# Performance work log

Measured on AMD Instinct MI355X. Metric: run time of the kernel, lower is better.

## Reference

```python
import jax, jax.numpy as jnp
import numpy as np

B, H, E, L = 2048, 4096, 8, 512
TAU = 1.0


def setup_inputs() -> dict:
    key = jax.random.key(0)
    k1, k2, k3, k4 = jax.random.split(key, 4)
    hidden = jax.random.normal(k1, (B, H), dtype=jnp.float32)
    envs = jax.random.normal(k2, (B, E), dtype=jnp.float32)
    idx = jnp.arange(B, dtype=jnp.int64)
    gumbel = jax.random.gumbel(k3, (B, E), dtype=jnp.float32)
    W = jax.random.normal(k4, (E, L, H), dtype=jnp.float32) * (1.0 / np.sqrt(H))
    return {"hidden": hidden, "envs": envs, "idx": idx, "gumbel": gumbel, "W": W}


def _hard_gumbel_softmax(log_probs, gumbel, tau):
    # F.gumbel_softmax(log_probs, tau=1, hard=True) with pre-sampled gumbel noise
    y_soft = jax.nn.softmax((log_probs + gumbel) / tau, axis=-1)
    y_hard = jax.nn.one_hot(jnp.argmax(y_soft, axis=-1), y_soft.shape[-1], dtype=y_soft.dtype)
    # straight-through estimator
    return y_hard + y_soft - jax.lax.stop_gradient(y_soft)


def reference(hidden, envs, idx, gumbel, W):
    # gating: env = gumbel_softmax(log_softmax(envs[idx]))  -> [B, E]
    log_probs = jax.nn.log_softmax(envs[idx], axis=-1)
    env = _hard_gumbel_softmax(log_probs, gumbel, TAU)
    # per-expert logits: [B, E, L]; fuses the per-sample python loop
    expert_logits = jnp.einsum("bh,elh->bel", hidden, W)
    # gating combine: [B, L]
    logits = jnp.einsum("be,bel->bl", env, expert_logits)
    # variance penalty over expert weights
    W_mean = jnp.mean(W, axis=0)  # [L, H]
    diff_sq = jnp.sum((W - W_mean[None]) ** 2, axis=(1, 2))  # ||W_e - W_mean||_2^2 per expert
    l1 = jnp.sum(jnp.abs(W), axis=(1, 2))                    # ||W_e||_1 per expert
    loss_penalty = jnp.mean(diff_sq / (l1 ** 2))
    return logits, loss_penalty
```

## Files before the change

### kernel.cpp

```cpp
#include <hip/hip_runtime.h>
#include <hip/hip_bf16.h>

constexpr int B = 2048, H = 4096, E = 8, L = 512;
constexpr int LH = L * H;

typedef float f4v __attribute__((ext_vector_type(4)));
typedef short short8 __attribute__((ext_vector_type(8)));

constexpr int BT = 64;
constexpr int LT = 128;
constexpr int KT = 32;
constexpr int SK = 4;
constexpr int RTMAX = 6;
constexpr int NITER = (H / SK) / KT;

constexpr int NGEMM = 4 * 2 * 4 * 4 * RTMAX;
constexpr int NPEN = 2048;

constexpr int NGRID = NGEMM + NPEN;

constexpr size_t WS_COUNTS = 0;
constexpr size_t WS_ACCUM = 32;
constexpr size_t WS_ROWLIST = 96;
constexpr size_t WS_ZERO_BYTES = 96;

using as1_u32 = const __attribute__((address_space(1))) unsigned int;
using as3_u32 = __attribute__((address_space(3))) unsigned int;

static __device__ __forceinline__ void dma16(const float* g, float* lds) {
  __builtin_amdgcn_global_load_lds((as1_u32*)g, (as3_u32*)lds, 16, 0, 0);
}

static __device__ __forceinline__ unsigned pk2(float a, float b) {
  __hip_bfloat162 p = __float22bfloat162_rn(make_float2(a, b));
  unsigned u;
  __builtin_memcpy(&u, &p, 4);
  return u;
}

static __device__ __forceinline__ short8 cvt8(f4v lo, f4v hi) {
  union { short8 s; unsigned u[4]; } r;
  r.u[0] = pk2(lo.x, lo.y);
  r.u[1] = pk2(lo.z, lo.w);
  r.u[2] = pk2(hi.x, hi.y);
  r.u[3] = pk2(hi.z, hi.w);
  return r.s;
}

__global__ void gating_kernel(const float* __restrict__ envs,
                              const float* __restrict__ gumbel,
                              int* __restrict__ counts,
                              int* __restrict__ row_list) {
  int b = blockIdx.x * blockDim.x + threadIdx.x;
  if (b >= B) return;
  float zmax = -1e30f;
  int am = 0;
#pragma unroll
  for (int e = 0; e < E; ++e) {
    float z = envs[b * E + e] + gumbel[b * E + e];
    if (z > zmax) { zmax = z; am = e; }
  }
  int pos = atomicAdd(&counts[am], 1);
  row_list[am * B + pos] = b;
}

__launch_bounds__(256, 3)
__global__ void fused_kernel(const float* __restrict__ hidden,
                             const float* __restrict__ W,
                             const int* __restrict__ counts,
                             const int* __restrict__ row_list,
                             float* __restrict__ out,
                             float* __restrict__ accum) {
  const int id = blockIdx.x;
  const int t = threadIdx.x;

  __shared__ __align__(16) float AshF[2][BT * KT];
  __shared__ __align__(16) float BshF[2][LT * KT];
  __shared__ int rlsh[BT];
  __shared__ float red[4][16];

  const int grp = id / 11;
  const int rem = id - grp * 11;
  const bool is_gemm = (rem < 3);

  if (!is_gemm) {
    const int p = (grp * 8 + (rem - 3)) * 256 + t;

    float4 w[E];
    float mx = 0.f, my = 0.f, mz = 0.f, mw = 0.f;
#pragma unroll
    for (int e = 0; e < E; ++e) {
      w[e] = *(const float4*)(W + (size_t)e * LH + (size_t)p * 4);
      mx += w[e].x; my += w[e].y; mz += w[e].z; mw += w[e].w;
    }
    mx *= 0.125f; my *= 0.125f; mz *= 0.125f; mw *= 0.125f;

    float vals[16];
#pragma unroll
    for (int e = 0; e < E; ++e) {
      float dx = w[e].x - mx, dy = w[e].y - my, dz = w[e].z - mz,
            dw = w[e].w - mw;
      vals[e] = dx * dx + dy * dy + dz * dz + dw * dw;
      vals[8 + e] =
          fabsf(w[e].x) + fabsf(w[e].y) + fabsf(w[e].z) + fabsf(w[e].w);
    }
#pragma unroll
    for (int k = 0; k < 16; ++k) {
      float v = vals[k];
      for (int off = 32; off > 0; off >>= 1) v += __shfl_xor(v, off);
      vals[k] = v;
    }
    const int wv = t >> 6, lane = t & 63;
    if (lane == 0) {
#pragma unroll
      for (int k = 0; k < 16; ++k) red[wv][k] = vals[k];
    }
    __syncthreads();
    if (t < 16) {
      atomicAdd(&accum[t], red[0][t] + red[1][t] + red[2][t] + red[3][t]);
    }
    return;
  }

  const int gidx = grp * 3 + rem;
  const int lt = gidx & 3;
  const int ep = (gidx >> 2) & 1;
  const int sk = (gidx >> 3) & 3;
  const int eh = (gidx >> 5) & 3;
  const int rt = gidx >> 7;
  const int e = eh * 2 + ep;

  const int cnt = counts[e];
  const int rbase = rt * BT;
  if (rbase >= cnt) return;
  const int lbase = lt * LT;

  if (t < BT) {
    int rr = rbase + t;
    rlsh[t] = row_list[e * B + (rr < cnt ? rr : (cnt - 1))];
  }
  __syncthreads();

  const float* Wp = W + (size_t)e * LH + (size_t)lbase * H;

  const int wave = t >> 6;
  const int lane = t & 63;
  const int quad = lane >> 4;
  const int l16 = lane & 15;
  const int wm = (wave >> 1) * 32;
  const int wn = (wave & 1) * 64;

  const int kbeg = sk * (H / SK);
  const int srow = lane >> 3;
  const int sblk = lane & 7;
  const int gblk = sblk ^ srow;

  const float* sp[6];
  float* sl[2][6];
#pragma unroll
  for (int i = 0; i < 6; ++i) {
    int g = wave * 6 + i;
    if (g < 8) {
      int rr = g * 8 + srow;
      sp[i] = hidden + (size_t)rlsh[rr] * H + kbeg + gblk * 4;
      sl[0][i] = &AshF[0][g * 8 * KT];
      sl[1][i] = &AshF[1][g * 8 * KT];
    } else {
      int rb = (g - 8) * 8 + srow;
      sp[i] = Wp + (size_t)rb * H + kbeg + gblk * 4;
      sl[0][i] = &BshF[0][(g - 8) * 8 * KT];
      sl[1][i] = &BshF[1][(g - 8) * 8 * KT];
    }
  }

  auto stage = [&](int buf) {
#pragma unroll
    for (int i = 0; i < 6; ++i) {
      dma16(sp[i], sl[buf][i]);
      sp[i] += KT;
    }
  };

  const int r7 = l16 & 7;
  const int slo = (2 * quad) ^ r7;
  const int shi = slo ^ 1;

  f4v acc[2][4] = {};

  stage(0);

  for (int it = 0; it < NITER; ++it) {
    const int buf = it & 1;
    __syncthreads();
    if (it + 1 < NITER) stage(buf ^ 1);

    short8 af[2], bf[4];
#pragma unroll
    for (int i = 0; i < 2; ++i) {
      int ra = wm + i * 16 + l16;
      f4v lo = *(const f4v*)&AshF[buf][ra * KT + slo * 4];
      f4v hi = *(const f4v*)&AshF[buf][ra * KT + shi * 4];
      af[i] = cvt8(lo, hi);
    }
#pragma unroll
    for (int j = 0; j < 4; ++j) {
      int rb = wn + j * 16 + l16;
      f4v lo = *(const f4v*)&BshF[buf][rb * KT + slo * 4];
      f4v hi = *(const f4v*)&BshF[buf][rb * KT + shi * 4];
      bf[j] = cvt8(lo, hi);
    }
#pragma unroll
    for (int i = 0; i < 2; ++i)
#pragma unroll
      for (int j = 0; j < 4; ++j)
        acc[i][j] =
            __builtin_amdgcn_mfma_f32_16x16x32_bf16(af[i], bf[j], acc[i][j],
                                                    0, 0, 0);
  }

#pragma unroll
  for (int i = 0; i < 2; ++i) {
#pragma unroll
    for (int j = 0; j < 4; ++j) {
#pragma unroll
      for (int reg = 0; reg < 4; ++reg) {
        int rloc = wm + i * 16 + quad * 4 + reg;
        if (rbase + rloc < cnt) {
          int bidx = rlsh[rloc];
          atomicAdd(&out[(size_t)bidx * L + lbase + wn + j * 16 + l16],
                    acc[i][j][reg]);
        }
      }
    }
  }
}

__global__ void finalize_kernel(const float* __restrict__ accum,
                                float* __restrict__ out) {
  if (threadIdx.x == 0) {
    float loss = 0.f;
#pragma unroll
    for (int e = 0; e < E; ++e) {
      float l1 = accum[8 + e];
      loss += accum[e] / (l1 * l1);
    }
    out[(size_t)B * L] = loss * 0.125f;
  }
}

extern "C" void kernel_launch(void* const* d_in, const int* in_sizes, int n_in,
                              void* d_out, int out_size, void* d_ws, size_t ws_size,
                              hipStream_t stream) {
  (void)in_sizes; (void)n_in; (void)ws_size;
  const float* hidden = (const float*)d_in[0];
  const float* envs   = (const float*)d_in[1];
  const float* gumbel = (const float*)d_in[3];
  const float* W      = (const float*)d_in[4];
  float* out = (float*)d_out;

  char* ws = (char*)d_ws;
  int*   counts   = (int*)(ws + WS_COUNTS);
  float* accum    = (float*)(ws + WS_ACCUM);
  int*   row_list = (int*)(ws + WS_ROWLIST);

  (void)hipMemsetAsync(d_ws, 0, WS_ZERO_BYTES, stream);
  (void)hipMemsetAsync(d_out, 0, (size_t)out_size * sizeof(float), stream);

  gating_kernel<<<dim3(B / 256), dim3(256), 0, stream>>>(envs, gumbel, counts,
                                                         row_list);

  fused_kernel<<<dim3(NGRID), dim3(256), 0, stream>>>(hidden, W, counts,
                                                      row_list, out, accum);

  finalize_kernel<<<dim3(1), dim3(64), 0, stream>>>(accum, out);
}
```

Measured before the change: 195.1 us.

## Enlarge GEMM row tile and stage bf16 operands in padded LDS via registers

```diff
diff --git a/kernel.cpp b/kernel.cpp
--- a/kernel.cpp
+++ b/kernel.cpp
@@ -7,28 +7,24 @@
 typedef float f4v __attribute__((ext_vector_type(4)));
 typedef short short8 __attribute__((ext_vector_type(8)));
 
-constexpr int BT = 64;
-constexpr int LT = 128;
-constexpr int KT = 32;
+constexpr int BT = 128, LT = 128, KT = 32;
 constexpr int SK = 4;
-constexpr int RTMAX = 6;
+constexpr int RTMAX = 3;
 constexpr int NITER = (H / SK) / KT;
+constexpr int ROWE = 40;
 
 constexpr int NGEMM = 4 * 2 * 4 * 4 * RTMAX;
 constexpr int NPEN = 2048;
-
 constexpr int NGRID = NGEMM + NPEN;
+
 
 constexpr size_t WS_COUNTS = 0;
 constexpr size_t WS_ACCUM = 32;
 constexpr size_t WS_ROWLIST = 96;
 constexpr size_t WS_ZERO_BYTES = 96;
 
-using as1_u32 = const __attribute__((address_space(1))) unsigned int;
-using as3_u32 = __attribute__((address_space(3))) unsigned int;
-
-static __device__ __forceinline__ void dma16(const float* g, float* lds) {
-  __builtin_amdgcn_global_load_lds((as1_u32*)g, (as3_u32*)lds, 16, 0, 0);
+static __device__ __forceinline__ void lgkm_barrier() {
+  __asm__ __volatile__("s_waitcnt lgkmcnt(0)\n\ts_barrier" ::: "memory");
 }
 
 static __device__ __forceinline__ unsigned pk2(float a, float b) {
@@ -36,15 +32,6 @@
   unsigned u;
   __builtin_memcpy(&u, &p, 4);
   return u;
-}
-
-static __device__ __forceinline__ short8 cvt8(f4v lo, f4v hi) {
-  union { short8 s; unsigned u[4]; } r;
-  r.u[0] = pk2(lo.x, lo.y);
-  r.u[1] = pk2(lo.z, lo.w);
-  r.u[2] = pk2(hi.x, hi.y);
-  r.u[3] = pk2(hi.z, hi.w);
-  return r.s;
 }
 
 __global__ void gating_kernel(const float* __restrict__ envs,
@@ -74,17 +61,16 @@
   const int id = blockIdx.x;
   const int t = threadIdx.x;
 
-  __shared__ __align__(16) float AshF[2][BT * KT];
-  __shared__ __align__(16) float BshF[2][LT * KT];
+  __shared__ __align__(16) unsigned short Ash[2][BT * ROWE];
+  __shared__ __align__(16) unsigned short Bsh[2][LT * ROWE];
   __shared__ int rlsh[BT];
   __shared__ float red[4][16];
 
-  const int grp = id / 11;
-  const int rem = id - grp * 11;
-  const bool is_gemm = (rem < 3);
-
-  if (!is_gemm) {
-    const int p = (grp * 8 + (rem - 3)) * 256 + t;
+  const int grp = id / 19;
+  const int rem = id - grp * 19;
+
+  if (rem >= 3) {
+    const int p = (grp * 16 + (rem - 3)) * 256 + t;
 
     float4 w[E];
     float mx = 0.f, my = 0.f, mz = 0.f, mw = 0.f;
@@ -147,79 +133,79 @@
   const int lane = t & 63;
   const int quad = lane >> 4;
   const int l16 = lane & 15;
-  const int wm = (wave >> 1) * 32;
+  const int wm = (wave >> 1) * 64;
   const int wn = (wave & 1) * 64;
 
+  const int srow = t >> 1;
+  const int sh = t & 1;
   const int kbeg = sk * (H / SK);
-  const int srow = lane >> 3;
-  const int sblk = lane & 7;
-  const int gblk = sblk ^ srow;
-
-  const float* sp[6];
-  float* sl[2][6];
-#pragma unroll
-  for (int i = 0; i < 6; ++i) {
-    int g = wave * 6 + i;
-    if (g < 8) {
-      int rr = g * 8 + srow;
-      sp[i] = hidden + (size_t)rlsh[rr] * H + kbeg + gblk * 4;
-      sl[0][i] = &AshF[0][g * 8 * KT];
-      sl[1][i] = &AshF[1][g * 8 * KT];
-    } else {
-      int rb = (g - 8) * 8 + srow;
-      sp[i] = Wp + (size_t)rb * H + kbeg + gblk * 4;
-      sl[0][i] = &BshF[0][(g - 8) * 8 * KT];
-      sl[1][i] = &BshF[1][(g - 8) * 8 * KT];
-    }
-  }
-
-  auto stage = [&](int buf) {
-#pragma unroll
-    for (int i = 0; i < 6; ++i) {
-      dma16(sp[i], sl[buf][i]);
-      sp[i] += KT;
+  const float* agp = hidden + (size_t)rlsh[srow] * H + kbeg + sh * 16;
+  const float* bgp = Wp + (size_t)srow * H + kbeg + sh * 16;
+  unsigned short* const alds[2] = {&Ash[0][srow * ROWE + sh * 16],
+                                   &Ash[1][srow * ROWE + sh * 16]};
+  unsigned short* const blds[2] = {&Bsh[0][srow * ROWE + sh * 16],
+                                   &Bsh[1][srow * ROWE + sh * 16]};
+
+  float4 ar[4], br[4];
+  auto issue_loads = [&](int k) {
+#pragma unroll
+    for (int i = 0; i < 4; ++i) {
+      ar[i] = *(const float4*)(agp + k + i * 4);
+      br[i] = *(const float4*)(bgp + k + i * 4);
     }
   };
-
-  const int r7 = l16 & 7;
-  const int slo = (2 * quad) ^ r7;
-  const int shi = slo ^ 1;
-
-  f4v acc[2][4] = {};
-
-  stage(0);
+  auto commit = [&](int buf) {
+    uint4 a0, a1, b0, b1;
+    a0.x = pk2(ar[0].x, ar[0].y); a0.y = pk2(ar[0].z, ar[0].w);
+    a0.z = pk2(ar[1].x, ar[1].y); a0.w = pk2(ar[1].z, ar[1].w);
+    a1.x = pk2(ar[2].x, ar[2].y); a1.y = pk2(ar[2].z, ar[2].w);
+    a1.z = pk2(ar[3].x, ar[3].y); a1.w = pk2(ar[3].z, ar[3].w);
+    b0.x = pk2(br[0].x, br[0].y); b0.y = pk2(br[0].z, br[0].w);
+    b0.z = pk2(br[1].x, br[1].y); b0.w = pk2(br[1].z, br[1].w);
+    b1.x = pk2(br[2].x, br[2].y); b1.y = pk2(br[2].z, br[2].w);
+    b1.z = pk2(br[3].x, br[3].y); b1.w = pk2(br[3].z, br[3].w);
+    *(uint4*)(alds[buf]) = a0;
+    *(uint4*)(alds[buf] + 8) = a1;
+    *(uint4*)(blds[buf]) = b0;
+    *(uint4*)(blds[buf] + 8) = b1;
+  };
+
+  f4v acc[4][4] = {};
+
+  issue_loads(0);
+  commit(0);
+  issue_loads(KT);
+  lgkm_barrier();
 
   for (int it = 0; it < NITER; ++it) {
     const int buf = it & 1;
-    __syncthreads();
-    if (it + 1 < NITER) stage(buf ^ 1);
-
-    short8 af[2], bf[4];
-#pragma unroll
-    for (int i = 0; i < 2; ++i) {
-      int ra = wm + i * 16 + l16;
-      f4v lo = *(const f4v*)&AshF[buf][ra * KT + slo * 4];
-      f4v hi = *(const f4v*)&AshF[buf][ra * KT + shi * 4];
-      af[i] = cvt8(lo, hi);
-    }
-#pragma unroll
-    for (int j = 0; j < 4; ++j) {
-      int rb = wn + j * 16 + l16;
-      f4v lo = *(const f4v*)&BshF[buf][rb * KT + slo * 4];
-      f4v hi = *(const f4v*)&BshF[buf][rb * KT + shi * 4];
-      bf[j] = cvt8(lo, hi);
-    }
-#pragma unroll
-    for (int i = 0; i < 2; ++i)
+
+    short8 af[4], bfr[4];
+#pragma unroll
+    for (int i = 0; i < 4; ++i)
+      af[i] = *(const short8*)&Ash[buf][(wm + i * 16 + l16) * ROWE + quad * 8];
+#pragma unroll
+    for (int j = 0; j < 4; ++j)
+      bfr[j] = *(const short8*)&Bsh[buf][(wn + j * 16 + l16) * ROWE + quad * 8];
+
+    if (it + 1 < NITER) {
+      commit(buf ^ 1);
+      if (it + 2 < NITER) issue_loads((it + 2) * KT);
+    }
+
+#pragma unroll
+    for (int i = 0; i < 4; ++i)
 #pragma unroll
       for (int j = 0; j < 4; ++j)
         acc[i][j] =
-            __builtin_amdgcn_mfma_f32_16x16x32_bf16(af[i], bf[j], acc[i][j],
+            __builtin_amdgcn_mfma_f32_16x16x32_bf16(af[i], bfr[j], acc[i][j],
                                                     0, 0, 0);
-  }
-
-#pragma unroll
-  for (int i = 0; i < 2; ++i) {
+
+    if (it + 1 < NITER) lgkm_barrier();
+  }
+
+#pragma unroll
+  for (int i = 0; i < 4; ++i) {
 #pragma unroll
     for (int j = 0; j < 4; ++j) {
 #pragma unroll
```

After: 213.4 us. 9.4% more time.
